# Kernel tuning notes

Measured on AMD Instinct MI355X. Metric: run time of the kernel, lower is better.

## Reference

```python
import jax, jax.numpy as jnp
import numpy as np

HIDDEN = 2048
NUM_HEADS = 6
HEAD_V = 512          # head_dim * expand_v = 256 * 2
VALUE_DIM = NUM_HEADS * HEAD_V  # 3072
CONV_K = 4
PHASE_BASE = 10000.0
EPS = 1e-5


def _causal_depthwise_conv(x, w):
    # x: [B, T, C], w: [C, K]; causal depthwise conv, no bias, no activation
    B, T, C = x.shape
    K = w.shape[1]
    xp = jnp.pad(x, ((0, 0), (K - 1, 0), (0, 0)))
    y = jnp.zeros_like(x)
    for j in range(K):
        y = y + xp[:, j:j + T, :] * w[:, j]
    return y


def _rotate(x, ang):
    # x: [..., D] interleaved RoPE pairs, ang: [..., D//2] pair angles
    cos = jnp.cos(ang)
    sin = jnp.sin(ang)
    xe = x[..., ::2]
    xo = x[..., 1::2]
    ye = xe * cos - xo * sin
    yo = xo * cos + xe * sin
    return jnp.stack([ye, yo], axis=-1).reshape(x.shape)


def setup_inputs() -> dict:
    key = jax.random.key(0)
    ks = jax.random.split(key, 12)
    s = 0.02
    return {
        "hidden_states": jax.random.normal(ks[0], (2, 2048, HIDDEN), jnp.float32),
        "Wq": jax.random.normal(ks[1], (HIDDEN, VALUE_DIM), jnp.float32) * s,
        "Wk": jax.random.normal(ks[2], (HIDDEN, VALUE_DIM), jnp.float32) * s,
        "Wv": jax.random.normal(ks[3], (HIDDEN, VALUE_DIM), jnp.float32) * s,
        "Wa": jax.random.normal(ks[4], (HIDDEN, NUM_HEADS), jnp.float32) * s,
        "Wb": jax.random.normal(ks[5], (HIDDEN, NUM_HEADS), jnp.float32) * s,
        "Wg": jax.random.normal(ks[6], (HIDDEN, VALUE_DIM), jnp.float32) * s,
        "Wo": jax.random.normal(ks[7], (VALUE_DIM, HIDDEN), jnp.float32) * s,
        "conv_q": jax.random.normal(ks[8], (VALUE_DIM, CONV_K), jnp.float32) * s,
        "conv_k": jax.random.normal(ks[9], (VALUE_DIM, CONV_K), jnp.float32) * s,
        "conv_v": jax.random.normal(ks[10], (VALUE_DIM, CONV_K), jnp.float32) * s,
        "rms_w": jnp.ones((HEAD_V,), jnp.float32),
    }


def _forward(hidden_states, Wq, Wk, Wv, Wa, Wb, Wg, Wo, conv_q, conv_k, conv_v, rms_w):
    B, T, _ = hidden_states.shape
    H, D = NUM_HEADS, HEAD_V
    inv_freq = 1.0 / (PHASE_BASE ** (jnp.arange(0, D, 2, dtype=jnp.float32) / D))  # [D/2]

    q = _causal_depthwise_conv(hidden_states @ Wq, conv_q).reshape(B, T, H, D)
    k = _causal_depthwise_conv(hidden_states @ Wk, conv_k).reshape(B, T, H, D)
    v = _causal_depthwise_conv(hidden_states @ Wv, conv_v).reshape(B, T, H, D)

    # pair angles (RoPE-style): raw even channels scaled by inverse frequencies
    theta = q[..., ::2] * inv_freq           # [B, T, H, D/2] output/query phase
    psi = k[..., ::2] * inv_freq             # write phase
    # state rotation per step = phase increment so cumulative state phase tracks theta
    phi = theta - jnp.concatenate([jnp.zeros_like(theta[:, :1]), theta[:, :-1]], axis=1)

    alpha = jax.nn.sigmoid(hidden_states @ Wa)  # [B, T, H] decay gate
    beta = jax.nn.sigmoid(hidden_states @ Wb)   # [B, T, H] write gate

    # time-major scan inputs
    tm = lambda a: jnp.moveaxis(a, 1, 0)
    xs = (tm(theta), tm(psi), tm(phi), tm(v), tm(alpha), tm(beta))

    def step(state, inp):
        th, ps, ph, vt, at, bt = inp  # state: [B, H, D]
        retained = _rotate(state, ph) * at[..., None]
        write = _rotate(vt, ps)
        new_state = retained + bt[..., None] * write
        out_t = _rotate(new_state, -th)
        return new_state, out_t

    state0 = jnp.zeros((B, H, D), hidden_states.dtype)
    _, out = jax.lax.scan(step, state0, xs)     # out: [T, B, H, D]
    out = jnp.moveaxis(out, 0, 1)               # [B, T, H, D]

    # gated RMSNorm over head_v_dim, then output projection
    g = (hidden_states @ Wg).reshape(B, T, H, D)
    rms = jax.lax.rsqrt(jnp.mean(jnp.square(out), axis=-1, keepdims=True) + EPS)
    o = out * rms * rms_w * jax.nn.silu(g)
    return (o.reshape(B, T, VALUE_DIM) @ Wo)


def reference(hidden_states, Wq, Wk, Wv, Wa, Wb, Wg, Wo, conv_q, conv_k, conv_v, rms_w):
    return _forward(hidden_states, Wq, Wk, Wv, Wa, Wb, Wg, Wo, conv_q, conv_k, conv_v, rms_w)
```

## Files before the change

kernel.cpp:

```cpp
#include <hip/hip_runtime.h>
#include <hip/hip_bf16.h>
#include <stdint.h>

using bf16 = __hip_bfloat16;
using mfrag = __attribute__((ext_vector_type(8))) __bf16;
using f32x4 = __attribute__((ext_vector_type(4))) float;

#define TOKENS 4096
#define HID    2048
#define VD     3072
#define NH     6
#define HD     512
#define NPAIR  256
#define N1     9216
#define NC     64
#define CHUNK  32

__device__ __forceinline__ void gld_lds16(const bf16* g, bf16* l) {
    __builtin_amdgcn_global_load_lds((const __attribute__((address_space(1))) void*)g,
                                     (__attribute__((address_space(3))) void*)l, 16, 0, 0);
}

#define VMWAIT(n) asm volatile("s_waitcnt vmcnt(" #n ")" ::: "memory")
#define SCHED0    __builtin_amdgcn_sched_barrier(0)
#define SBAR      __builtin_amdgcn_s_barrier()

template<int BN_T>
__global__ __launch_bounds__(512, 2) void k_gemm5(const bf16* __restrict__ A,
                                                  const bf16* __restrict__ Bt,
                                                  void* __restrict__ Cv,
                                                  int M, int N, int K, int obf,
                                                  int n0, int nbn) {
    constexpr int WN   = (BN_T == 256) ? 4 : 2;
    constexpr int WM   = 8 / WN;
    constexpr int MF   = (256 / WM) / 16;
    constexpr int AQ   = MF / 4;
    constexpr int SH   = AQ * 16;
    constexpr int NHT  = 2 + BN_T / 128;
    constexpr int HT   = 16384;
    constexpr int SLOT = NHT * HT;

    extern __shared__ char smem[];
    const int tid  = threadIdx.x;
    const int wave = tid >> 6;
    const int lane = tid & 63;
    const int lrow = lane & 15;
    const int lk   = lane >> 4;
    const int wm   = wave / WN;
    const int wn   = wave % WN;

    const int bid = blockIdx.x;
    const int xcd = bid & 7;
    const int kk2 = bid >> 3;
    const int rn  = nbn >> 1;
    const int jj  = kk2 & 31;
    const int bm  = ((((xcd >> 1) << 2) + (jj & 3)) << 8);
    const int bn  = ((xcd & 1) * rn + (kk2 >> 5) * 8 + (jj >> 2)) * BN_T;

    const int NT = K >> 6;

    auto ST_B = [&](int half, int t) {
        char* sb = smem + (size_t)(t & 1) * SLOT + (2 + half) * HT;
        const int ko = t << 6;
#pragma unroll
        for (int i = 0; i < 2; ++i) {
            const int L = i * 512 + tid;
            const int r = L >> 3;
            const int c = (L & 7) ^ (r & 7);
            gld_lds16(Bt + (size_t)(bn + half * 128 + r) * K + ko + c * 8,
                      (bf16*)(sb + (size_t)L * 16));
        }
    };
    auto ST_A = [&](int unit, int t) {
        char* sb = smem + (size_t)(t & 1) * SLOT;
        const int ko = t << 6;
        const int s  = tid / (SH * 8);
        const int W  = tid % (SH * 8);
        const int rl = W >> 3;
        const int c  = W & 7;
        const int r256 = s * (256 / WM) + unit * SH + rl;
        const int cl = c ^ (r256 & 7);
        const int ht = r256 >> 7, lr = r256 & 127;
        gld_lds16(A + (size_t)(bm + r256) * K + ko + cl * 8,
                  (bf16*)(sb + (size_t)ht * HT + (size_t)lr * 128 + c * 16));
    };

    auto rdA = [&](const char* rb, int mf, int kk) -> mfrag {
        const int r  = wm * (MF * 16) + mf * 16 + lrow;
        const int ht = r >> 7, lr = r & 127;
        const int cc = (kk * 4 + lk) ^ (lr & 7);
        return *(const mfrag*)(rb + (size_t)ht * HT + (size_t)lr * 128 + cc * 16);
    };
    auto rdB = [&](const char* rb, int nf, int kk) -> mfrag {
        const int r  = wn * 64 + nf * 16 + lrow;
        const int ht = r >> 7, lr = r & 127;
        const int cc = (kk * 4 + lk) ^ (lr & 7);
        return *(const mfrag*)(rb + (size_t)(2 + ht) * HT + (size_t)lr * 128 + cc * 16);
    };

    f32x4 acc[MF][4];
#pragma unroll
    for (int m = 0; m < MF; ++m)
#pragma unroll
        for (int n = 0; n < 4; ++n) acc[m][n] = f32x4{0.f, 0.f, 0.f, 0.f};

    ST_B(0, 0);
    if (BN_T == 256) ST_B(1, 0);
    ST_A(0, 0); ST_A(1, 0); ST_A(2, 0); ST_A(3, 0);

#define RD_A(AF, band)                                                          \
    _Pragma("unroll")                                                           \
    for (int i = 0; i < AQ; ++i)                                                \
        _Pragma("unroll")                                                       \
        for (int kx = 0; kx < 2; ++kx) AF[i][kx] = rdA(rb, (band) * AQ + i, kx);

#define MFMA_Q(q, AF)                                                           \
    __builtin_amdgcn_s_setprio(1);                                              \
    _Pragma("unroll")                                                           \
    for (int i = 0; i < AQ; ++i)                                                \
        _Pragma("unroll")                                                       \
        for (int nf = 0; nf < 4; ++nf) {                                        \
            const int mi = (q) * AQ + i;                                        \
            acc[mi][nf] = __builtin_amdgcn_mfma_f32_16x16x32_bf16(AF[i][0], bfr[nf][0], acc[mi][nf], 0, 0, 0); \
            acc[mi][nf] = __builtin_amdgcn_mfma_f32_16x16x32_bf16(AF[i][1], bfr[nf][1], acc[mi][nf], 0, 0, 0); \
        }                                                                       \
    __builtin_amdgcn_s_setprio(0);

    for (int kt = 0; kt < NT; ++kt) {
        const char* rb = smem + (size_t)(kt & 1) * SLOT;
        const bool last = (kt == NT - 1);
        mfrag bfr[4][2];
        mfrag af0[AQ][2], af1[AQ][2], af2[AQ][2], af3[AQ][2];

        VMWAIT(2);
        SCHED0; SBAR;
#pragma unroll
        for (int nf = 0; nf < 4; ++nf)
#pragma unroll
            for (int kx = 0; kx < 2; ++kx) bfr[nf][kx] = rdB(rb, nf, kx);
        RD_A(af0, 0)
        if (!last) ST_B(0, kt + 1);
        RD_A(af1, 1)
        SCHED0;
        MFMA_Q(0, af0)

        if (last) { VMWAIT(1); } else { VMWAIT(3); }
        SCHED0; SBAR;
        if (!last) {
            if (BN_T == 256) ST_B(1, kt + 1);
            else             { ST_A(0, kt + 1); ST_A(1, kt + 1); }
        }
        RD_A(af2, 2)
        SCHED0;
        MFMA_Q(1, af1)

        if (last) { VMWAIT(0); } else { VMWAIT(4); }
        SCHED0; SBAR;
        if (!last) {
            if (BN_T == 256) { ST_A(0, kt + 1); ST_A(1, kt + 1); }
            else             { ST_A(2, kt + 1); ST_A(3, kt + 1); }
        }
        RD_A(af3, 3)
        SCHED0;
        MFMA_Q(2, af2)

        SBAR;
        if (!last && BN_T == 256) { ST_A(2, kt + 1); ST_A(3, kt + 1); }
        SCHED0;
        MFMA_Q(3, af3)
    }
#undef RD_A
#undef MFMA_Q

#pragma unroll
    for (int m = 0; m < MF; ++m)
#pragma unroll
        for (int j2 = 0; j2 < 4; ++j2) {
            const int r = bm + wm * (MF * 16) + m * 16 + lk * 4 + j2;
#pragma unroll
            for (int n = 0; n < 4; ++n) {
                const int c = n0 + bn + wn * 64 + n * 16 + lrow;
                if (obf) ((bf16*)Cv)[(size_t)r * N + c] = __float2bfloat16(acc[m][n][j2]);
                else     ((float*)Cv)[(size_t)r * N + c] = acc[m][n][j2];
            }
        }
}

__global__ void k_prep_w(const float* __restrict__ Wq, const float* __restrict__ Wk,
                         const float* __restrict__ Wv, const float* __restrict__ Wg,
                         bf16* __restrict__ Wt) {
    __shared__ float t[32][33];
    const int n0 = blockIdx.x * 32;
    const int k0 = blockIdx.y * 32;
    const int tx = threadIdx.x, ty = threadIdx.y;
    const float* src; int cb, cs;
    if (n0 < 1536)      { int m = n0;        src = Wq; cb = (m >> 8) * 512 + (m & 255) * 2; cs = 2; }
    else if (n0 < 3072) { int m = n0 - 1536; src = Wk; cb = (m >> 8) * 512 + (m & 255) * 2; cs = 2; }
    else if (n0 < 6144) { int m = n0 - 3072; src = Wv; cb = m; cs = 1; }
    else                { int m = n0 - 6144; src = Wg; cb = m; cs = 1; }
#pragma unroll
    for (int i = 0; i < 4; ++i) {
        int k = k0 + ty + i * 8;
        t[ty + i * 8][tx] = src[(size_t)k * VD + cb + cs * tx];
    }
    __syncthreads();
#pragma unroll
    for (int i = 0; i < 4; ++i) {
        int n = n0 + ty + i * 8;
        Wt[(size_t)n * HID + k0 + tx] = __float2bfloat16(t[tx][ty + i * 8]);
    }
}

__global__ void k_tr_cast(const float* __restrict__ src, bf16* __restrict__ dst, int R, int Ccol) {
    __shared__ float t[32][33];
    const int c0 = blockIdx.x * 32, r0 = blockIdx.y * 32;
    const int tx = threadIdx.x, ty = threadIdx.y;
#pragma unroll
    for (int i = 0; i < 4; ++i)
        t[ty + i * 8][tx] = src[(size_t)(r0 + ty + i * 8) * Ccol + c0 + tx];
    __syncthreads();
#pragma unroll
    for (int i = 0; i < 4; ++i)
        dst[(size_t)(c0 + ty + i * 8) * R + r0 + tx] = __float2bfloat16(t[tx][ty + i * 8]);
}

__global__ __launch_bounds__(256) void k_ab(const float* __restrict__ hs, const float* __restrict__ Wa,
                                            const float* __restrict__ Wb,
                                            float* __restrict__ alpha, float* __restrict__ beta,
                                            bf16* __restrict__ hsb) {
    const int tok = blockIdx.x;
    const int tid = threadIdx.x;
    float part[12];
#pragma unroll
    for (int j = 0; j < 12; ++j) part[j] = 0.f;
    const float* hrow = hs + (size_t)tok * HID;
    bf16* hbrow = hsb + (size_t)tok * HID;
    for (int i = 0; i < 8; ++i) {
        int k = i * 256 + tid;
        float x = hrow[k];
        hbrow[k] = __float2bfloat16(x);
        const float* wa = Wa + k * NH;
        const float* wb = Wb + k * NH;
#pragma unroll
        for (int j = 0; j < NH; ++j) {
            part[j]     = fmaf(x, wa[j], part[j]);
            part[6 + j] = fmaf(x, wb[j], part[6 + j]);
        }
    }
    __shared__ float red[12][4];
    const int lane = tid & 63, wv = tid >> 6;
#pragma unroll
    for (int j = 0; j < 12; ++j) {
        float s = part[j];
        for (int off = 32; off; off >>= 1) s += __shfl_down(s, off);
        if (lane == 0) red[j][wv] = s;
    }
    __syncthreads();
    if (tid < 12) {
        float s = red[tid][0] + red[tid][1] + red[tid][2] + red[tid][3];
        float v = 1.f / (1.f + expf(-s));
        if (tid < 6) alpha[(size_t)tok * NH + tid] = v;
        else         beta [(size_t)tok * NH + tid - 6] = v;
    }
}

__global__ __launch_bounds__(256) void k_scan1(const bf16* __restrict__ X,
                                               const float* __restrict__ alpha,
                                               const float* __restrict__ beta,
                                               const float* __restrict__ cq,
                                               const float* __restrict__ ck,
                                               const float* __restrict__ cv,
                                               bf16* __restrict__ U, float* __restrict__ pp) {
    const int bx = blockIdx.x;
    const int c  = bx % NC;
    const int h  = (bx / NC) % NH;
    const int b  = bx / (NC * NH);
    const int p  = threadIdx.x;
    const int t0 = c * CHUNK;
    const int ch2 = h * HD + 2 * p;
    const float wq0 = cq[ch2 * 4 + 0], wq1 = cq[ch2 * 4 + 1], wq2 = cq[ch2 * 4 + 2], wq3 = cq[ch2 * 4 + 3];
    const float wk0 = ck[ch2 * 4 + 0], wk1 = ck[ch2 * 4 + 1], wk2 = ck[ch2 * 4 + 2], wk3 = ck[ch2 * 4 + 3];
    const float wa0 = cv[ch2 * 4 + 0], wa1 = cv[ch2 * 4 + 1], wa2 = cv[ch2 * 4 + 2], wa3 = cv[ch2 * 4 + 3];
    const float wb0 = cv[(ch2 + 1) * 4 + 0], wb1 = cv[(ch2 + 1) * 4 + 1],
                wb2 = cv[(ch2 + 1) * 4 + 2], wb3 = cv[(ch2 + 1) * 4 + 3];
    const float invf = exp2f(-13.287712379549449f * ((float)p * (1.0f / 256.0f)));
    const int qcol = h * NPAIR + p;
    const int kcol = 1536 + h * NPAIR + p;
    const int vcol = 3072 + ch2;

    float xq[3], xk[3], xv0[3], xv1[3];
#pragma unroll
    for (int i = 0; i < 3; ++i) {
        int t = t0 - 3 + i;
        if (t >= 0) {
            size_t tok = (size_t)b * 2048 + t;
            const bf16* xr = X + tok * N1;
            xq[i] = __bfloat162float(xr[qcol]);
            xk[i] = __bfloat162float(xr[kcol]);
            __hip_bfloat162 vv = *(const __hip_bfloat162*)&xr[vcol];
            xv0[i] = __bfloat162float(vv.x);
            xv1[i] = __bfloat162float(vv.y);
        } else { xq[i] = xk[i] = xv0[i] = xv1[i] = 0.f; }
    }

    float u0 = 0.f, u1 = 0.f, ap = 1.f;
    for (int t = t0; t < t0 + CHUNK; ++t) {
        const size_t tok = (size_t)b * 2048 + t;
        const bf16* xr = X + tok * N1;
        float nq = __bfloat162float(xr[qcol]);
        float nk = __bfloat162float(xr[kcol]);
        __hip_bfloat162 vv = *(const __hip_bfloat162*)&xr[vcol];
        float nv0 = __bfloat162float(vv.x);
        float nv1 = __bfloat162float(vv.y);
        float yq  = wq3 * nq  + wq2 * xq[2]  + wq1 * xq[1]  + wq0 * xq[0];
        float yk  = wk3 * nk  + wk2 * xk[2]  + wk1 * xk[1]  + wk0 * xk[0];
        float yv0 = wa3 * nv0 + wa2 * xv0[2] + wa1 * xv0[1] + wa0 * xv0[0];
        float yv1 = wb3 * nv1 + wb2 * xv1[2] + wb1 * xv1[1] + wb0 * xv1[0];
        xq[0] = xq[1]; xq[1] = xq[2]; xq[2] = nq;
        xk[0] = xk[1]; xk[1] = xk[2]; xk[2] = nk;
        xv0[0] = xv0[1]; xv0[1] = xv0[2]; xv0[2] = nv0;
        xv1[0] = xv1[1]; xv1[1] = xv1[2]; xv1[2] = nv1;
        float theta = yq * invf, psi = yk * invf;
        float d = psi - theta, sn, cs;
        __sincosf(d, &sn, &cs);
        float w0 = yv0 * cs - yv1 * sn;
        float w1 = yv1 * cs + yv0 * sn;
        float a  = alpha[tok * NH + h];
        float bb = beta [tok * NH + h];
        u0 = fmaf(a, u0, bb * w0);
        u1 = fmaf(a, u1, bb * w1);
        ap *= a;
        __hip_bfloat162 us;
        us.x = __float2bfloat16(u0);
        us.y = __float2bfloat16(u1);
        *(__hip_bfloat162*)&U[tok * (size_t)VD + h * HD + 2 * p] = us;
        if (p == 0) pp[tok * NH + h] = ap;
    }
}

__global__ __launch_bounds__(512) void k_carry(const bf16* __restrict__ U, const float* __restrict__ pp,
                                               float* __restrict__ carry) {
    const int bh = blockIdx.x;
    const int b = bh / NH, h = bh % NH;
    const int d = threadIdx.x;
    float ue[NC], pv[NC];
#pragma unroll
    for (int c = 0; c < NC; ++c) {
        size_t tok = (size_t)b * 2048 + c * CHUNK + CHUNK - 1;
        ue[c] = __bfloat162float(U[tok * (size_t)VD + h * HD + d]);
        pv[c] = pp[tok * NH + h];
    }
    float s = 0.f;
#pragma unroll
    for (int c = 0; c < NC; ++c) {
        carry[((size_t)bh * NC + c) * HD + d] = s;
        s = ue[c] + pv[c] * s;
    }
}

__global__ __launch_bounds__(256) void k_pass3(const bf16* __restrict__ U, const float* __restrict__ pp,
                                               const float* __restrict__ carry, const bf16* __restrict__ X,
                                               const float* __restrict__ rms_w, bf16* __restrict__ O) {
    const int bx = blockIdx.x;
    const int h = bx % NH;
    const size_t tok = bx / NH;
    const int b = (int)(tok >> 11);
    const int t = (int)(tok & 2047);
    const int c = t / CHUNK;
    const int tid = threadIdx.x;
    const int d = tid * 2;
    __hip_bfloat162 uu2 = *(const __hip_bfloat162*)&U[tok * (size_t)VD + h * HD + d];
    float  P  = pp[tok * NH + h];
    float2 cy = *(const float2*)&carry[((size_t)(b * NH + h) * NC + c) * HD + d];
    float u0 = fmaf(P, cy.x, __bfloat162float(uu2.x));
    float u1 = fmaf(P, cy.y, __bfloat162float(uu2.y));
    float s = u0 * u0 + u1 * u1;
    for (int off = 32; off; off >>= 1) s += __shfl_down(s, off);
    __shared__ float r4[4];
    const int lane = tid & 63, wv = tid >> 6;
    if (lane == 0) r4[wv] = s;
    __syncthreads();
    float tot = r4[0] + r4[1] + r4[2] + r4[3];
    float rms = rsqrtf(tot * (1.f / 512.f) + 1e-5f);
    __hip_bfloat162 gg = *(const __hip_bfloat162*)&X[tok * N1 + 6144 + h * HD + d];
    float g0 = __bfloat162float(gg.x), g1 = __bfloat162float(gg.y);
    float si0 = g0 / (1.f + expf(-g0));
    float si1 = g1 / (1.f + expf(-g1));
    float o0 = u0 * rms * rms_w[d]     * si0;
    float o1 = u1 * rms * rms_w[d + 1] * si1;
    __hip_bfloat162 ob;
    ob.x = __float2bfloat16(o0);
    ob.y = __float2bfloat16(o1);
    *(__hip_bfloat162*)&O[tok * (size_t)VD + h * HD + d] = ob;
}

extern "C" void kernel_launch(void* const* d_in, const int* in_sizes, int n_in,
                              void* d_out, int out_size, void* d_ws, size_t ws_size,
                              hipStream_t stream) {
    const float* hs   = (const float*)d_in[0];
    const float* Wq   = (const float*)d_in[1];
    const float* Wk   = (const float*)d_in[2];
    const float* Wv   = (const float*)d_in[3];
    const float* Wa   = (const float*)d_in[4];
    const float* Wb   = (const float*)d_in[5];
    const float* Wg   = (const float*)d_in[6];
    const float* Wo   = (const float*)d_in[7];
    const float* cq   = (const float*)d_in[8];
    const float* ck   = (const float*)d_in[9];
    const float* cv   = (const float*)d_in[10];
    const float* rmsw = (const float*)d_in[11];

    char* ws = (char*)d_ws;
    size_t off = 0;
    auto alloc = [&](size_t bytes) -> void* {
        void* p = ws + off;
        off = (off + bytes + 255) & ~(size_t)255;
        return p;
    };
    bf16*  hsb   = (bf16*) alloc((size_t)TOKENS * HID * 2);
    bf16*  Wt    = (bf16*) alloc((size_t)N1 * HID * 2);
    bf16*  Wot   = (bf16*) alloc((size_t)HID * VD * 2);
    bf16*  X     = (bf16*) alloc((size_t)TOKENS * N1 * 2);
    bf16*  U     = (bf16*) alloc((size_t)TOKENS * VD * 2);
    float* alp   = (float*)alloc((size_t)TOKENS * NH * 4);
    float* bet   = (float*)alloc((size_t)TOKENS * NH * 4);
    float* pp    = (float*)alloc((size_t)TOKENS * NH * 4);
    float* carry = (float*)alloc((size_t)2 * NH * NC * HD * 4);
    bf16*  O     = (bf16*)Wt;

    hipFuncSetAttribute((const void*)k_gemm5<256>,
                        hipFuncAttributeMaxDynamicSharedMemorySize, 2 * 4 * 16384);
    hipFuncSetAttribute((const void*)k_gemm5<128>,
                        hipFuncAttributeMaxDynamicSharedMemorySize, 2 * 3 * 16384);

    k_prep_w<<<dim3(N1 / 32, HID / 32), dim3(32, 8), 0, stream>>>(Wq, Wk, Wv, Wg, Wt);
    k_tr_cast<<<dim3(HID / 32, VD / 32), dim3(32, 8), 0, stream>>>(Wo, Wot, VD, HID);
    k_ab<<<TOKENS, 256, 0, stream>>>(hs, Wa, Wb, alp, bet, hsb);
    k_gemm5<256><<<dim3(512), 512, 2 * 4 * 16384, stream>>>(hsb, Wt, X, TOKENS, N1, HID, 1, 0, 32);
    k_gemm5<128><<<dim3(128), 512, 2 * 3 * 16384, stream>>>(hsb, Wt + (size_t)8192 * HID, X,
                                                            TOKENS, N1, HID, 1, 8192, 8);
    k_scan1<<<2 * NH * NC, 256, 0, stream>>>(X, alp, bet, cq, ck, cv, U, pp);
    k_carry<<<2 * NH, 512, 0, stream>>>(U, pp, carry);
    k_pass3<<<TOKENS * NH, 256, 0, stream>>>(U, pp, carry, X, rmsw, O);
    k_gemm5<128><<<dim3(256), 512, 2 * 3 * 16384, stream>>>(O, Wot, d_out, TOKENS, HID, VD, 0, 0, 16);
}
```

Baseline: 343.6 us.

## Halve scan chunk size and map one wavefront per token-head in pass3

Chunk length drops from 32 to 16, doubling the number of chunks, so the sequential intra-chunk scan launches twice as many blocks with half the serial depth. The carry kernel now loads chunk endpoints in batches of 32 to keep register use bounded at the larger chunk count. The normalize/gate kernel assigns each (token, head) row to a single 64-lane wavefront that handles 8 elements per lane, which removes the shared-memory reduction and block barrier. The cost is a longer serial carry pass and more carry data to write and read.

```diff
diff --git a/kernel.cpp b/kernel.cpp
--- a/kernel.cpp
+++ b/kernel.cpp
@@ -13,8 +13,8 @@
 #define HD     512
 #define NPAIR  256
 #define N1     9216
-#define NC     64
-#define CHUNK  32
+#define NC     128
+#define CHUNK  16
 
 __device__ __forceinline__ void gld_lds16(const bf16* g, bf16* l) {
     __builtin_amdgcn_global_load_lds((const __attribute__((address_space(1))) void*)g,
@@ -343,55 +343,67 @@
     const int bh = blockIdx.x;
     const int b = bh / NH, h = bh % NH;
     const int d = threadIdx.x;
-    float ue[NC], pv[NC];
-#pragma unroll
-    for (int c = 0; c < NC; ++c) {
-        size_t tok = (size_t)b * 2048 + c * CHUNK + CHUNK - 1;
-        ue[c] = __bfloat162float(U[tok * (size_t)VD + h * HD + d]);
-        pv[c] = pp[tok * NH + h];
-    }
     float s = 0.f;
-#pragma unroll
-    for (int c = 0; c < NC; ++c) {
-        carry[((size_t)bh * NC + c) * HD + d] = s;
-        s = ue[c] + pv[c] * s;
+    for (int cb = 0; cb < NC; cb += 32) {
+        float ue[32], pv[32];
+#pragma unroll
+        for (int i = 0; i < 32; ++i) {
+            size_t tok = (size_t)b * 2048 + (cb + i) * CHUNK + CHUNK - 1;
+            ue[i] = __bfloat162float(U[tok * (size_t)VD + h * HD + d]);
+            pv[i] = pp[tok * NH + h];
+        }
+#pragma unroll
+        for (int i = 0; i < 32; ++i) {
+            carry[((size_t)bh * NC + cb + i) * HD + d] = s;
+            s = ue[i] + pv[i] * s;
+        }
     }
 }
 
 __global__ __launch_bounds__(256) void k_pass3(const bf16* __restrict__ U, const float* __restrict__ pp,
                                                const float* __restrict__ carry, const bf16* __restrict__ X,
                                                const float* __restrict__ rms_w, bf16* __restrict__ O) {
-    const int bx = blockIdx.x;
-    const int h = bx % NH;
-    const size_t tok = bx / NH;
+    const int r    = blockIdx.x * 4 + (threadIdx.x >> 6);
+    const int lane = threadIdx.x & 63;
+    const size_t tok = r / NH;
+    const int h = r % NH;
     const int b = (int)(tok >> 11);
     const int t = (int)(tok & 2047);
     const int c = t / CHUNK;
-    const int tid = threadIdx.x;
-    const int d = tid * 2;
-    __hip_bfloat162 uu2 = *(const __hip_bfloat162*)&U[tok * (size_t)VD + h * HD + d];
-    float  P  = pp[tok * NH + h];
-    float2 cy = *(const float2*)&carry[((size_t)(b * NH + h) * NC + c) * HD + d];
-    float u0 = fmaf(P, cy.x, __bfloat162float(uu2.x));
-    float u1 = fmaf(P, cy.y, __bfloat162float(uu2.y));
-    float s = u0 * u0 + u1 * u1;
-    for (int off = 32; off; off >>= 1) s += __shfl_down(s, off);
-    __shared__ float r4[4];
-    const int lane = tid & 63, wv = tid >> 6;
-    if (lane == 0) r4[wv] = s;
-    __syncthreads();
-    float tot = r4[0] + r4[1] + r4[2] + r4[3];
-    float rms = rsqrtf(tot * (1.f / 512.f) + 1e-5f);
-    __hip_bfloat162 gg = *(const __hip_bfloat162*)&X[tok * N1 + 6144 + h * HD + d];
-    float g0 = __bfloat162float(gg.x), g1 = __bfloat162float(gg.y);
-    float si0 = g0 / (1.f + expf(-g0));
-    float si1 = g1 / (1.f + expf(-g1));
-    float o0 = u0 * rms * rms_w[d]     * si0;
-    float o1 = u1 * rms * rms_w[d + 1] * si1;
-    __hip_bfloat162 ob;
-    ob.x = __float2bfloat16(o0);
-    ob.y = __float2bfloat16(o1);
-    *(__hip_bfloat162*)&O[tok * (size_t)VD + h * HD + d] = ob;
+    const size_t ubase = tok * (size_t)VD + h * HD;
+    const size_t cbase = ((size_t)(b * NH + h) * NC + c) * HD;
+    const float P = pp[tok * NH + h];
+
+    float u0v[4], u1v[4];
+    float s = 0.f;
+#pragma unroll
+    for (int i = 0; i < 4; ++i) {
+        const int pi = lane + i * 64;
+        __hip_bfloat162 uu = *(const __hip_bfloat162*)&U[ubase + 2 * pi];
+        float2 cy = *(const float2*)&carry[cbase + 2 * pi];
+        float u0 = fmaf(P, cy.x, __bfloat162float(uu.x));
+        float u1 = fmaf(P, cy.y, __bfloat162float(uu.y));
+        u0v[i] = u0; u1v[i] = u1;
+        s = fmaf(u0, u0, s);
+        s = fmaf(u1, u1, s);
+    }
+#pragma unroll
+    for (int off = 32; off; off >>= 1) s += __shfl_xor(s, off);
+    const float rms = rsqrtf(s * (1.f / 512.f) + 1e-5f);
+
+#pragma unroll
+    for (int i = 0; i < 4; ++i) {
+        const int pi = lane + i * 64;
+        __hip_bfloat162 gg = *(const __hip_bfloat162*)&X[tok * N1 + 6144 + h * HD + 2 * pi];
+        float g0 = __bfloat162float(gg.x), g1 = __bfloat162float(gg.y);
+        float si0 = g0 / (1.f + expf(-g0));
+        float si1 = g1 / (1.f + expf(-g1));
+        float2 rw = *(const float2*)&rms_w[2 * pi];
+        __hip_bfloat162 ob;
+        ob.x = __float2bfloat16(u0v[i] * rms * rw.x * si0);
+        ob.y = __float2bfloat16(u1v[i] * rms * rw.y * si1);
+        *(__hip_bfloat162*)&O[ubase + 2 * pi] = ob;
+    }
 }
 
 extern "C" void kernel_launch(void* const* d_in, const int* in_sizes, int n_in,
@@ -441,6 +453,6 @@
                                                             TOKENS, N1, HID, 1, 8192, 8);
     k_scan1<<<2 * NH * NC, 256, 0, stream>>>(X, alp, bet, cq, ck, cv, U, pp);
     k_carry<<<2 * NH, 512, 0, stream>>>(U, pp, carry);
-    k_pass3<<<TOKENS * NH, 256, 0, stream>>>(U, pp, carry, X, rmsw, O);
+    k_pass3<<<TOKENS * NH / 4, 256, 0, stream>>>(U, pp, carry, X, rmsw, O);
     k_gemm5<128><<<dim3(256), 512, 2 * 3 * 16384, stream>>>(O, Wot, d_out, TOKENS, HID, VD, 0, 0, 16);
 }
```

Result: faster. 325.3 us (-5.3%).
